# Performance work log

Measured on AMD Instinct MI355X. Metric: run time of the kernel, lower is better.

The kernel has to match this reference:

```python
import jax, jax.numpy as jnp
import numpy as np

N, n, d = 4, 2048, 1024


def setup_inputs() -> dict:
    key = jax.random.key(0)
    k1, k2, k3, k4 = jax.random.split(key, 4)
    x = jax.random.normal(k1, (N, n, d), dtype=jnp.float32)
    mask = jax.random.randint(k2, (N, n, n), 0, 2, dtype=jnp.int32)
    Wqk = jax.random.normal(k3, (d, d), dtype=jnp.float32) * (d ** -0.5)
    Wvc = jax.random.normal(k4, (d, d), dtype=jnp.float32) * (d ** -0.5)
    return {"x": x, "mask": mask, "Wqk": Wqk, "Wvc": Wvc}


def reference(x, mask, Wqk, Wvc):
    # q = Wqk(x): torch Linear computes x @ W^T
    q = jnp.einsum('bnd,ed->bne', x, Wqk)          # [N, n, d]
    scale = jnp.asarray(x.shape[-1], x.dtype) ** 0.5
    scores = jnp.einsum('bnd,bmd->bnm', q, x) / scale  # [N, n, n]
    scores = jnp.where(mask == 0, jnp.asarray(-1e20, scores.dtype), scores)
    attention = jax.nn.softmax(scores, axis=-1)
    attended = jnp.einsum('bnm,bmd->bnd', attention, x)
    return jnp.einsum('bnd,ed->bne', attended, Wvc)
```

## Files before the change

kernel.cpp:

```cpp
#include <hip/hip_runtime.h>
#include <hip/hip_bf16.h>

typedef short bf16x8 __attribute__((ext_vector_type(8)));
typedef short s16x4  __attribute__((ext_vector_type(4)));
typedef short s16x8  __attribute__((ext_vector_type(8)));
typedef float f32x4  __attribute__((ext_vector_type(4)));

static __device__ __forceinline__ void async_cp16(const void* g, void* l) {
  __builtin_amdgcn_global_load_lds(
      (const __attribute__((address_space(1))) unsigned int*)g,
      (__attribute__((address_space(3))) unsigned int*)l, 16, 0, 0);
}

static __device__ __forceinline__ unsigned short f2bf_bits(float f) {
  union { __hip_bfloat16 b; unsigned short u; } cv;
  cv.b = __float2bfloat16(f);
  return cv.u;
}
static __device__ __forceinline__ float bf2f(short u) {
  union { float f; unsigned v; } cv;
  cv.v = ((unsigned)(unsigned short)u) << 16;
  return cv.f;
}

#define BAR() __builtin_amdgcn_s_barrier()
#define SBZ() __builtin_amdgcn_sched_barrier(0)
#define VMW(n) do { asm volatile("s_waitcnt vmcnt(" #n ")" ::: "memory"); SBZ(); } while (0)

__global__ __launch_bounds__(256) void cvt_all(const float* __restrict__ x,
                                               const float* __restrict__ wqk,
                                               const float* __restrict__ wvc,
                                               __hip_bfloat16* __restrict__ xb,
                                               __hip_bfloat16* __restrict__ wqkb,
                                               __hip_bfloat16* __restrict__ wvcb) {
  const int b = blockIdx.x;
  const float* in;
  __hip_bfloat16* out;
  long base;
  if (b < 8192)       { in = x;   out = xb;   base = (long)b * 1024; }
  else if (b < 9216)  { in = wqk; out = wqkb; base = (long)(b - 8192) * 1024; }
  else                { in = wvc; out = wvcb; base = (long)(b - 9216) * 1024; }
  const long i = base + threadIdx.x * 4;
  const float4 v = *(const float4*)(in + i);
  s16x4 o;
  o[0] = (short)f2bf_bits(v.x);
  o[1] = (short)f2bf_bits(v.y);
  o[2] = (short)f2bf_bits(v.z);
  o[3] = (short)f2bf_bits(v.w);
  *(s16x4*)(out + i) = o;
}

struct GemmDesc {
  const __hip_bfloat16* A; const __hip_bfloat16* B; void* C;
  int lda, ldb, ldc, nT, tpb; long sA, sB, sC; float cscale;
};

template<int MODE>
__global__ __launch_bounds__(512, 2) void gemm4b(GemmDesc g0, GemmDesc g1, int nb0, int K) {
  constexpr int BOFF  = 16384;
  constexpr int BUFSZ = 32768;
  __shared__ char lds[4 * BUFSZ];

  const int bid = blockIdx.x, nwg = gridDim.x;
  const int wg = (bid & 7) * (nwg >> 3) + (bid >> 3);
  GemmDesc g = (wg < nb0) ? g0 : g1;
  const int id = (wg < nb0) ? wg : wg - nb0;
  const int bz = id / g.tpb, tl = id - bz * g.tpb;
  const int bm = tl / g.nT, bn = tl - bm * g.nT;
  const long m0 = (long)bm * 256, n0 = (long)bn * 256;
  const __hip_bfloat16* Ab = g.A + bz * g.sA;
  const __hip_bfloat16* Bb = g.B + bz * g.sB;

  const int t = threadIdx.x;
  const int lane = t & 63, w = t >> 6;
  const int wm = w >> 2, wn = w & 3;
  const int lr = lane & 15, cs = lane >> 4;

  const int rA  = t >> 2;
  const int dsl = t & 3;
  const int ssl = dsl ^ ((rA >> 1) & 3);
  const __hip_bfloat16* aSt0 = Ab + (m0 + rA) * g.lda + ssl * 8;
  const __hip_bfloat16* aSt1 = Ab + (m0 + 128 + rA) * g.lda + ssl * 8;
  const __hip_bfloat16* bSt0 = Bb + (n0 + rA) * g.ldb + ssl * 8;
  const __hip_bfloat16* bSt1 = Bb + (n0 + 128 + rA) * g.ldb + ssl * 8;

  const int axor = ((lr >> 1) & 3) << 4;
  int aRd[8], bRd[4];
  #pragma unroll
  for (int mm = 0; mm < 8; ++mm)
    aRd[mm] = (wm * 128 + mm * 16 + lr) * 64 + ((cs << 4) ^ axor);
  #pragma unroll
  for (int nf = 0; nf < 4; ++nf)
    bRd[nf] = BOFF + (wn * 64 + nf * 16 + lr) * 64 + ((cs << 4) ^ axor);

  f32x4 acc[8][4] = {};

  #define STAGE(kt, base) do { \
    async_cp16(aSt0 + (long)(kt) * 32, lds + (base) + t * 16); \
    async_cp16(aSt1 + (long)(kt) * 32, lds + (base) + 8192 + t * 16); \
    async_cp16(bSt0 + (long)(kt) * 32, lds + (base) + BOFF + t * 16); \
    async_cp16(bSt1 + (long)(kt) * 32, lds + (base) + BOFF + 8192 + t * 16); \
  } while (0)

  const int nt = K >> 5;
  STAGE(0, 0);
  STAGE(1, BUFSZ);
  STAGE(2, 2 * BUFSZ);
  VMW(8);
  BAR();

  int rb = 0, sb = 3 * BUFSZ;
  for (int tt = 0; tt < nt; ++tt) {
    bf16x8 af[8], bq[4];
    #pragma unroll
    for (int mm = 0; mm < 8; ++mm)
      af[mm] = *(const bf16x8*)(lds + rb + aRd[mm]);
    #pragma unroll
    for (int nf = 0; nf < 4; ++nf)
      bq[nf] = *(const bf16x8*)(lds + rb + bRd[nf]);
    if (tt + 3 < nt) STAGE(tt + 3, sb);
    #pragma unroll
    for (int mm = 0; mm < 8; ++mm)
      #pragma unroll
      for (int nf = 0; nf < 4; ++nf)
        acc[mm][nf] = __builtin_amdgcn_mfma_f32_16x16x32_bf16(af[mm], bq[nf], acc[mm][nf], 0, 0, 0);
    if (tt + 3 < nt) { VMW(8); } else { VMW(0); }
    BAR();
    rb = (rb == 3 * BUFSZ) ? 0 : rb + BUFSZ;
    sb = (sb == 3 * BUFSZ) ? 0 : sb + BUFSZ;
  }
  #undef STAGE

  const long crow0 = m0 + wm * 128 + cs * 4;
  const long ccol0 = n0 + wn * 64 + lr;
  if (MODE == 0) {
    float* C = (float*)g.C + bz * g.sC;
    #pragma unroll
    for (int mm = 0; mm < 8; ++mm)
      #pragma unroll
      for (int nf = 0; nf < 4; ++nf)
        #pragma unroll
        for (int rr = 0; rr < 4; ++rr)
          C[(crow0 + mm * 16 + rr) * g.ldc + ccol0 + nf * 16] = acc[mm][nf][rr];
  } else {
    __hip_bfloat16* C = (__hip_bfloat16*)g.C + bz * g.sC;
    #pragma unroll
    for (int mm = 0; mm < 8; ++mm)
      #pragma unroll
      for (int nf = 0; nf < 4; ++nf)
        #pragma unroll
        for (int rr = 0; rr < 4; ++rr)
          C[(crow0 + mm * 16 + rr) * g.ldc + ccol0 + nf * 16] =
              __float2bfloat16(acc[mm][nf][rr] * g.cscale);
  }
}

template<int MODE, int BM_, int BK_>
__global__ __launch_bounds__(1024, 4) void gemm16(GemmDesc g0, GemmDesc g1, int nb0, int K) {
  constexpr int MR = BM_ / 64;
  constexpr int KR = BK_ / 32;
  constexpr int W  = BK_ * 2;
  constexpr int NB = (256 * W) / 16384;
  constexpr int BUFSZ = 16384 + NB * 16384;
  constexpr int KW = 1 + NB;
  __shared__ char lds[3 * BUFSZ];

  const int bid = blockIdx.x, nwg = gridDim.x;
  const int wg = (bid & 7) * (nwg >> 3) + (bid >> 3);
  GemmDesc g = (wg < nb0) ? g0 : g1;
  const int id = (wg < nb0) ? wg : wg - nb0;
  const int bz = id / g.tpb, tl = id - bz * g.tpb;
  const int bm = tl / g.nT, bn = tl - bm * g.nT;
  const long m0 = (long)bm * BM_, n0 = (long)bn * 256;
  const __hip_bfloat16* Ab = g.A + bz * g.sA;
  const __hip_bfloat16* Bb = g.B + bz * g.sB;

  const int t = threadIdx.x;
  const int lane = t & 63, w = t >> 6;
  const int wm = w >> 2, wn = w & 3;
  const int lr = lane & 15, cs = lane >> 4;

  const int rA  = t / (W / 16);
  const int dsl = t % (W / 16);
  const int ssl = dsl ^ ((W == 64) ? ((rA >> 1) & 3) : (rA & 7));
  const __hip_bfloat16* aSt  = Ab + (m0 + rA) * g.lda + ssl * 8;
  const __hip_bfloat16* bSt0 = Bb + (n0 + rA) * g.ldb + ssl * 8;
  const __hip_bfloat16* bSt1 = Bb + (n0 + 128 + rA) * g.ldb + ssl * 8;

  const int axor = (W == 64) ? (((lr >> 1) & 3) << 4) : ((lr & 7) << 4);
  int aRd[MR][KR], bRd[4][KR];
  #pragma unroll
  for (int mm = 0; mm < MR; ++mm)
    #pragma unroll
    for (int ks = 0; ks < KR; ++ks)
      aRd[mm][ks] = (wm * (BM_ / 4) + mm * 16 + lr) * W + ((((ks * 4 + cs) << 4) ^ axor));
  #pragma unroll
  for (int nf = 0; nf < 4; ++nf)
    #pragma unroll
    for (int ks = 0; ks < KR; ++ks)
      bRd[nf][ks] = 16384 + (wn * 64 + nf * 16 + lr) * W + ((((ks * 4 + cs) << 4) ^ axor));

  f32x4 acc[MR][4] = {};

  #define STAGE(kt, base) do { \
    async_cp16(aSt + (long)(kt) * BK_, lds + (base) + t * 16); \
    async_cp16(bSt0 + (long)(kt) * BK_, lds + (base) + 16384 + t * 16); \
    if (NB == 2) async_cp16(bSt1 + (long)(kt) * BK_, lds + (base) + 32768 + t * 16); \
  } while (0)
  #define VM_KW() do { if constexpr (KW == 2) { VMW(2); } else { VMW(3); } } while (0)

  const int nt = K / BK_;
  STAGE(0, 0);
  STAGE(1, BUFSZ);
  VM_KW();
  BAR();

  int rb = 0, sb = 2 * BUFSZ;
  for (int tt = 0; tt < nt; ++tt) {
    bf16x8 af[MR][KR], bq[4][KR];
    #pragma unroll
    for (int mm = 0; mm < MR; ++mm)
      #pragma unroll
      for (int ks = 0; ks < KR; ++ks)
        af[mm][ks] = *(const bf16x8*)(lds + rb + aRd[mm][ks]);
    #pragma unroll
    for (int nf = 0; nf < 4; ++nf)
      #pragma unroll
      for (int ks = 0; ks < KR; ++ks)
        bq[nf][ks] = *(const bf16x8*)(lds + rb + bRd[nf][ks]);
    if (tt + 2 < nt) STAGE(tt + 2, sb);
    #pragma unroll
    for (int ks = 0; ks < KR; ++ks)
      #pragma unroll
      for (int mm = 0; mm < MR; ++mm)
        #pragma unroll
        for (int nf = 0; nf < 4; ++nf)
          acc[mm][nf] = __builtin_amdgcn_mfma_f32_16x16x32_bf16(af[mm][ks], bq[nf][ks], acc[mm][nf], 0, 0, 0);
    if (tt + 2 < nt) { VM_KW(); } else { VMW(0); }
    BAR();
    rb = (rb == 2 * BUFSZ) ? 0 : rb + BUFSZ;
    sb = (sb == 2 * BUFSZ) ? 0 : sb + BUFSZ;
  }
  #undef STAGE
  #undef VM_KW

  const long crow0 = m0 + wm * (BM_ / 4) + cs * 4;
  const long ccol0 = n0 + wn * 64 + lr;
  if (MODE == 0) {
    float* C = (float*)g.C + bz * g.sC;
    #pragma unroll
    for (int mm = 0; mm < MR; ++mm)
      #pragma unroll
      for (int nf = 0; nf < 4; ++nf)
        #pragma unroll
        for (int rr = 0; rr < 4; ++rr)
          C[(crow0 + mm * 16 + rr) * g.ldc + ccol0 + nf * 16] = acc[mm][nf][rr];
  } else {
    __hip_bfloat16* C = (__hip_bfloat16*)g.C + bz * g.sC;
    #pragma unroll
    for (int mm = 0; mm < MR; ++mm)
      #pragma unroll
      for (int nf = 0; nf < 4; ++nf)
        #pragma unroll
        for (int rr = 0; rr < 4; ++rr)
          C[(crow0 + mm * 16 + rr) * g.ldc + ccol0 + nf * 16] =
              __float2bfloat16(acc[mm][nf][rr] * g.cscale);
  }
}

__global__ __launch_bounds__(256) void softmax_rows(__hip_bfloat16* __restrict__ S,
                                                    const int* __restrict__ Mask) {
  const long row = blockIdx.x;
  short* srow = (short*)(S + row * 2048);
  const int* mrow = Mask + row * 2048;
  const int t = threadIdx.x;
  const s16x8 sv = *(const s16x8*)(srow + t * 8);
  const int4 q0 = *(const int4*)(mrow + t * 8);
  const int4 q1 = *(const int4*)(mrow + t * 8 + 4);
  const int mk[8] = {q0.x, q0.y, q0.z, q0.w, q1.x, q1.y, q1.z, q1.w};

  float e[8];
  float s = 0.f;
  #pragma unroll
  for (int i = 0; i < 8; ++i) {
    e[i] = mk[i] ? __expf(bf2f(sv[i])) : 0.f;
    s += e[i];
  }
  #pragma unroll
  for (int off = 32; off > 0; off >>= 1) s += __shfl_xor(s, off);
  __shared__ float reds[4];
  if ((t & 63) == 0) reds[t >> 6] = s;
  __syncthreads();
  s = reds[0] + reds[1] + reds[2] + reds[3];

  s16x8 o;
  if (s > 0.f) {
    const float inv = 1.f / s;
    #pragma unroll
    for (int i = 0; i < 8; ++i) o[i] = (short)f2bf_bits(e[i] * inv);
  } else {
    const unsigned short u = f2bf_bits(1.f / 2048.f);
    #pragma unroll
    for (int i = 0; i < 8; ++i) o[i] = (short)u;
  }
  *(s16x8*)(srow + t * 8) = o;
}

extern "C" void kernel_launch(void* const* d_in, const int* in_sizes, int n_in,
                              void* d_out, int out_size, void* d_ws, size_t ws_size,
                              hipStream_t stream) {
  const float* x   = (const float*)d_in[0];
  const int*   msk = (const int*)d_in[1];
  const float* Wqk = (const float*)d_in[2];
  const float* Wvc = (const float*)d_in[3];
  float* out = (float*)d_out;
  char* ws = (char*)d_ws;

  __hip_bfloat16* xb   = (__hip_bfloat16*)(ws + 0);
  __hip_bfloat16* qb   = (__hip_bfloat16*)(ws + 16777216);
  __hip_bfloat16* vT   = (__hip_bfloat16*)(ws + 33554432);
  __hip_bfloat16* wqkb = (__hip_bfloat16*)(ws + 50331648);
  __hip_bfloat16* wvcb = (__hip_bfloat16*)(ws + 52428800);
  __hip_bfloat16* Sbf  = (__hip_bfloat16*)(ws + 54525952);

  cvt_all<<<dim3(10240), 256, 0, stream>>>(x, Wqk, Wvc, xb, wqkb, wvcb);

  GemmDesc gq{xb,   wqkb, qb, 1024, 1024, 1024, 4, 128, 0L, 0L, 0L, 0.03125f};
  GemmDesc gv{wvcb, xb,   vT, 1024, 1024, 2048, 8, 32, 0L, 2097152L, 2097152L, 1.f};
  gemm4b<1><<<dim3(256), 512, 0, stream>>>(gq, gv, 128, 1024);

  GemmDesc gs{qb, xb, Sbf, 1024, 1024, 2048, 8, 64, 2097152L, 2097152L, 4194304L, 1.f};
  gemm4b<1><<<dim3(256), 512, 0, stream>>>(gs, gs, 256, 1024);

  softmax_rows<<<dim3(8192), 256, 0, stream>>>(Sbf, msk);

  GemmDesc go{Sbf, vT, out, 2048, 2048, 1024, 4, 64, 4194304L, 2097152L, 2097152L, 1.f};
  gemm16<0, 128, 64><<<dim3(256), 1024, 0, stream>>>(go, go, 256, 2048);
}
```

Baseline: 141.5 us.

## Use 1024-thread GEMM with B operand read directly from global memory

Replaces the 512-thread 256x256 GEMM used for the Q/V and score products with a 1024-thread variant. Only the A tile is staged through LDS, with triple buffering instead of quad, while each wave loads its B fragments straight from global memory into registers. Each wave now holds a 64x64 accumulator instead of 128x64, which lowers register pressure and LDS footprint. The trade-off is uncached, non-shared global loads of B on every K step, duplicated across the waves that share those columns, and global load latency is exposed inside the loop.

Measured after the change: 207.5 us. 1.47x slower.

```diff
diff --git a/kernel.cpp b/kernel.cpp
--- a/kernel.cpp
+++ b/kernel.cpp
@@ -56,10 +56,9 @@
 };
 
 template<int MODE>
-__global__ __launch_bounds__(512, 2) void gemm4b(GemmDesc g0, GemmDesc g1, int nb0, int K) {
-  constexpr int BOFF  = 16384;
-  constexpr int BUFSZ = 32768;
-  __shared__ char lds[4 * BUFSZ];
+__global__ __launch_bounds__(1024, 4) void gemmfl(GemmDesc g0, GemmDesc g1, int nb0, int K) {
+  constexpr int BUFSZ = 16384;
+  __shared__ char lds[3 * BUFSZ];
 
   const int bid = blockIdx.x, nwg = gridDim.x;
   const int wg = (bid & 7) * (nwg >> 3) + (bid >> 3);
@@ -79,64 +78,56 @@
   const int rA  = t >> 2;
   const int dsl = t & 3;
   const int ssl = dsl ^ ((rA >> 1) & 3);
-  const __hip_bfloat16* aSt0 = Ab + (m0 + rA) * g.lda + ssl * 8;
-  const __hip_bfloat16* aSt1 = Ab + (m0 + 128 + rA) * g.lda + ssl * 8;
-  const __hip_bfloat16* bSt0 = Bb + (n0 + rA) * g.ldb + ssl * 8;
-  const __hip_bfloat16* bSt1 = Bb + (n0 + 128 + rA) * g.ldb + ssl * 8;
+  const __hip_bfloat16* aSt = Ab + (m0 + rA) * g.lda + ssl * 8;
 
   const int axor = ((lr >> 1) & 3) << 4;
-  int aRd[8], bRd[4];
-  #pragma unroll
-  for (int mm = 0; mm < 8; ++mm)
-    aRd[mm] = (wm * 128 + mm * 16 + lr) * 64 + ((cs << 4) ^ axor);
+  int aRd[4];
+  #pragma unroll
+  for (int mm = 0; mm < 4; ++mm)
+    aRd[mm] = (wm * 64 + mm * 16 + lr) * 64 + ((cs << 4) ^ axor);
+
+  const __hip_bfloat16* bP[4];
   #pragma unroll
   for (int nf = 0; nf < 4; ++nf)
-    bRd[nf] = BOFF + (wn * 64 + nf * 16 + lr) * 64 + ((cs << 4) ^ axor);
-
-  f32x4 acc[8][4] = {};
-
-  #define STAGE(kt, base) do { \
-    async_cp16(aSt0 + (long)(kt) * 32, lds + (base) + t * 16); \
-    async_cp16(aSt1 + (long)(kt) * 32, lds + (base) + 8192 + t * 16); \
-    async_cp16(bSt0 + (long)(kt) * 32, lds + (base) + BOFF + t * 16); \
-    async_cp16(bSt1 + (long)(kt) * 32, lds + (base) + BOFF + 8192 + t * 16); \
-  } while (0)
+    bP[nf] = Bb + (n0 + wn * 64 + nf * 16 + lr) * (long)g.ldb + cs * 8;
+
+  f32x4 acc[4][4] = {};
+
+  #define STAGE(kt, base) async_cp16(aSt + (long)(kt) * 32, lds + (base) + t * 16)
 
   const int nt = K >> 5;
   STAGE(0, 0);
   STAGE(1, BUFSZ);
-  STAGE(2, 2 * BUFSZ);
-  VMW(8);
-  BAR();
-
-  int rb = 0, sb = 3 * BUFSZ;
+  VMW(1);
+  BAR(); SBZ();
+
+  int rb = 0, sb = 2 * BUFSZ;
   for (int tt = 0; tt < nt; ++tt) {
-    bf16x8 af[8], bq[4];
-    #pragma unroll
-    for (int mm = 0; mm < 8; ++mm)
+    bf16x8 bq[4], af[4];
+    #pragma unroll
+    for (int nf = 0; nf < 4; ++nf)
+      bq[nf] = *(const bf16x8*)(bP[nf] + (long)tt * 32);
+    #pragma unroll
+    for (int mm = 0; mm < 4; ++mm)
       af[mm] = *(const bf16x8*)(lds + rb + aRd[mm]);
-    #pragma unroll
-    for (int nf = 0; nf < 4; ++nf)
-      bq[nf] = *(const bf16x8*)(lds + rb + bRd[nf]);
-    if (tt + 3 < nt) STAGE(tt + 3, sb);
-    #pragma unroll
-    for (int mm = 0; mm < 8; ++mm)
+    if (tt + 2 < nt) STAGE(tt + 2, sb);
+    #pragma unroll
+    for (int mm = 0; mm < 4; ++mm)
       #pragma unroll
       for (int nf = 0; nf < 4; ++nf)
         acc[mm][nf] = __builtin_amdgcn_mfma_f32_16x16x32_bf16(af[mm], bq[nf], acc[mm][nf], 0, 0, 0);
-    if (tt + 3 < nt) { VMW(8); } else { VMW(0); }
-    BAR();
-    rb = (rb == 3 * BUFSZ) ? 0 : rb + BUFSZ;
-    sb = (sb == 3 * BUFSZ) ? 0 : sb + BUFSZ;
+    BAR(); SBZ();
+    rb = (rb == 2 * BUFSZ) ? 0 : rb + BUFSZ;
+    sb = (sb == 2 * BUFSZ) ? 0 : sb + BUFSZ;
   }
   #undef STAGE
 
-  const long crow0 = m0 + wm * 128 + cs * 4;
+  const long crow0 = m0 + wm * 64 + cs * 4;
   const long ccol0 = n0 + wn * 64 + lr;
   if (MODE == 0) {
     float* C = (float*)g.C + bz * g.sC;
     #pragma unroll
-    for (int mm = 0; mm < 8; ++mm)
+    for (int mm = 0; mm < 4; ++mm)
       #pragma unroll
       for (int nf = 0; nf < 4; ++nf)
         #pragma unroll
@@ -145,7 +136,7 @@
   } else {
     __hip_bfloat16* C = (__hip_bfloat16*)g.C + bz * g.sC;
     #pragma unroll
-    for (int mm = 0; mm < 8; ++mm)
+    for (int mm = 0; mm < 4; ++mm)
       #pragma unroll
       for (int nf = 0; nf < 4; ++nf)
         #pragma unroll
@@ -327,10 +318,10 @@
 
   GemmDesc gq{xb,   wqkb, qb, 1024, 1024, 1024, 4, 128, 0L, 0L, 0L, 0.03125f};
   GemmDesc gv{wvcb, xb,   vT, 1024, 1024, 2048, 8, 32, 0L, 2097152L, 2097152L, 1.f};
-  gemm4b<1><<<dim3(256), 512, 0, stream>>>(gq, gv, 128, 1024);
+  gemmfl<1><<<dim3(256), 1024, 0, stream>>>(gq, gv, 128, 1024);
 
   GemmDesc gs{qb, xb, Sbf, 1024, 1024, 2048, 8, 64, 2097152L, 2097152L, 4194304L, 1.f};
-  gemm4b<1><<<dim3(256), 512, 0, stream>>>(gs, gs, 256, 1024);
+  gemmfl<1><<<dim3(256), 1024, 0, stream>>>(gs, gs, 256, 1024);
 
   softmax_rows<<<dim3(8192), 256, 0, stream>>>(Sbf, msk);
 
```
